# Performance work log

Hardware: AMD Instinct MI355X
Metric: run time of the kernel (lower is better)

Reference implementation:

```python
import jax, jax.numpy as jnp
import numpy as np

B, S, H, NH = 2, 2048, 1024, 16
HD = H // NH  # head_size = 64


def setup_inputs() -> dict:
    key = jax.random.key(0)
    ks = jax.random.split(key, 9)
    sc = 0.02
    return {
        "hidden_states": jax.random.normal(ks[0], (B, S, H), dtype=jnp.float32),
        "Wq": jax.random.normal(ks[1], (H, H), dtype=jnp.float32) * sc,
        "bq": jax.random.normal(ks[2], (H,), dtype=jnp.float32) * sc,
        "Wk": jax.random.normal(ks[3], (H, H), dtype=jnp.float32) * sc,
        "bk": jax.random.normal(ks[4], (H,), dtype=jnp.float32) * sc,
        "Wv": jax.random.normal(ks[5], (H, H), dtype=jnp.float32) * sc,
        "bv": jax.random.normal(ks[6], (H,), dtype=jnp.float32) * sc,
        "Wo": jax.random.normal(ks[7], (H, H), dtype=jnp.float32) * sc,
        "bo": jax.random.normal(ks[8], (H,), dtype=jnp.float32) * sc,
    }


def reference(hidden_states, Wq, bq, Wk, bk, Wv, bv, Wo, bo):
    b, s, h = hidden_states.shape
    # nn.Linear: y = x @ W.T + b
    q = hidden_states @ Wq.T + bq
    k = hidden_states @ Wk.T + bk
    v = hidden_states @ Wv.T + bv
    q = q.reshape(b, s, NH, HD)
    k = k.reshape(b, s, NH, HD)
    v = v.reshape(b, s, NH, HD)
    # scores: [b, heads, q, k]
    scores = jnp.einsum("bqhd,bkhd->bhqk", q, k) / jnp.sqrt(jnp.float32(HD))
    # causal mask: triu(ones, diagonal=1) positions set to -inf
    causal = jnp.triu(jnp.ones((s, s), dtype=bool), k=1)
    scores = jnp.where(causal[None, None], -jnp.inf, scores)
    attn = jax.nn.softmax(scores, axis=-1)
    ctx = jnp.einsum("bhqk,bkhd->bqhd", attn, v).reshape(b, s, h)
    return ctx @ Wo.T + bo
```

## Files before the change

kernel.cpp:

```cpp
#include <hip/hip_runtime.h>
#include <hip/hip_bf16.h>

#define B_  2
#define S_  2048
#define H_  1024
#define NH_ 16
#define HD_ 64

typedef unsigned short u16;
typedef unsigned int   u32;
typedef __attribute__((ext_vector_type(4)))  float  f32x4;
typedef __attribute__((ext_vector_type(16))) float  f32x16;
typedef __attribute__((ext_vector_type(8)))  __bf16 bf16x8;
typedef __attribute__((ext_vector_type(4)))  unsigned int u32x4;
typedef __attribute__((ext_vector_type(4)))  unsigned short u16x4;

__device__ __forceinline__ u16 f2bf(float f) {
  unsigned u = __builtin_bit_cast(unsigned, f);
  u += 0x7fffu + ((u >> 16) & 1u);
  return (u16)(u >> 16);
}
__device__ __forceinline__ u32 cvtpk(float lo, float hi) {
  u32 r;
  asm("v_cvt_pk_bf16_f32 %0, %1, %2" : "=v"(r) : "v"(lo), "v"(hi));
  return r;
}
__device__ __forceinline__ float ex2(float x) {
  float r;
  asm("v_exp_f32 %0, %1" : "=v"(r) : "v"(x));
  return r;
}

__device__ __forceinline__ void gload_lds16(const void* g, void* l) {
  __builtin_amdgcn_global_load_lds(
      (const __attribute__((address_space(1))) void*)g,
      (__attribute__((address_space(3))) void*)l, 16, 0, 0);
}

#define NX_ (4u * 1024u * 1024u)
__global__ __launch_bounds__(256) void cvt_all(const float* __restrict__ x,
                                               const float* __restrict__ w0, const float* __restrict__ w1,
                                               const float* __restrict__ w2, const float* __restrict__ w3,
                                               u16* __restrict__ xb,
                                               u16* __restrict__ o0, u16* __restrict__ o1,
                                               u16* __restrict__ o2, u16* __restrict__ o3) {
  size_t i4 = ((size_t)blockIdx.x * 256 + threadIdx.x) * 4;
  const float* src; u16* dst; size_t off;
  if (i4 < (size_t)NX_) { src = x; dst = xb; off = i4; }
  else {
    size_t j = i4 - NX_;
    int seg = (int)(j >> 20);
    off = j & ((1u << 20) - 1);
    src = seg == 0 ? w0 : seg == 1 ? w1 : seg == 2 ? w2 : w3;
    dst = seg == 0 ? o0 : seg == 1 ? o1 : seg == 2 ? o2 : o3;
  }
  float4 v = *reinterpret_cast<const float4*>(src + off);
  u16x4 o;
  o[0] = f2bf(v.x); o[1] = f2bf(v.y); o[2] = f2bf(v.z); o[3] = f2bf(v.w);
  *reinterpret_cast<u16x4*>(dst + off) = o;
}

__device__ __forceinline__ void store_out(float* C, size_t idx, float v) { C[idx] = v; }
__device__ __forceinline__ void store_out(u16* C, size_t idx, float v) { C[idx] = f2bf(v); }

template <int MI, typename OutT>
__device__ __forceinline__ void gemm_core(const u16* __restrict__ A, const u16* __restrict__ Bw,
                                          const float* __restrict__ bias, OutT* __restrict__ C,
                                          int M, int N, int K, float oscale, int m0, int n0,
                                          u16* lsA, u16* lsB) {
  const int t = threadIdx.x;
  const int w = t >> 6, lane = t & 63;
  const int g = lane >> 4, c = lane & 15;
  const int wr = w >> 1, wc = w & 1;

  f32x4 acc[MI][4] = {};
  const int rowS = w * 16 + (lane >> 2);
  const int colS = (lane & 3) * 8;

  for (int k0 = 0; k0 < K; k0 += 32) {
    __syncthreads();
#pragma unroll
    for (int r = 0; r < MI / 2; ++r)
      gload_lds16(A + (size_t)(m0 + r * 64 + rowS) * K + k0 + colS, lsA + r * 2048 + w * 512);
#pragma unroll
    for (int r = 0; r < 2; ++r)
      gload_lds16(Bw + (size_t)(n0 + r * 64 + rowS) * K + k0 + colS, lsB + r * 2048 + w * 512);
    asm volatile("s_waitcnt vmcnt(0)" ::: "memory");
    __syncthreads();

    bf16x8 af[MI], bfr[4];
#pragma unroll
    for (int mi = 0; mi < MI; ++mi)
      af[mi] = *reinterpret_cast<const bf16x8*>(&lsA[(wr * (MI * 16) + mi * 16 + c) * 32 + g * 8]);
#pragma unroll
    for (int ni = 0; ni < 4; ++ni)
      bfr[ni] = *reinterpret_cast<const bf16x8*>(&lsB[(wc * 64 + ni * 16 + c) * 32 + g * 8]);
#pragma unroll
    for (int mi = 0; mi < MI; ++mi)
#pragma unroll
      for (int ni = 0; ni < 4; ++ni)
        acc[mi][ni] = __builtin_amdgcn_mfma_f32_16x16x32_bf16(af[mi], bfr[ni], acc[mi][ni], 0, 0, 0);
  }

#pragma unroll
  for (int mi = 0; mi < MI; ++mi) {
    int rowb = m0 + wr * (MI * 16) + mi * 16 + g * 4;
#pragma unroll
    for (int ni = 0; ni < 4; ++ni) {
      int col = n0 + wc * 64 + ni * 16 + c;
      float bv = bias[col];
#pragma unroll
      for (int r = 0; r < 4; ++r) {
        float v = (acc[mi][ni][r] + bv) * oscale;
        store_out(C, (size_t)(rowb + r) * N + col, v);
      }
    }
  }
}

__global__ __launch_bounds__(256) void gemm_qkv(const u16* __restrict__ xb,
                                                const u16* __restrict__ Wq, const u16* __restrict__ Wk,
                                                const u16* __restrict__ Wv,
                                                const float* __restrict__ bq, const float* __restrict__ bk,
                                                const float* __restrict__ bv,
                                                u16* __restrict__ Q, u16* __restrict__ Kb, u16* __restrict__ Vb,
                                                int M, int K, float qscale) {
  __shared__ u16 lsA[4096];
  __shared__ u16 lsB[4096];
  const int fid = blockIdx.x;
  const int xcd = fid & 7, i = fid >> 3;
  const int mloc = i / 24, nn = i % 24;
  const int m0 = (xcd * 4 + mloc) * 128;
  const int ng = nn * 128;
  const int sel = ng >> 10, n0 = ng & 1023;
  const u16*  W    = sel == 0 ? Wq : sel == 1 ? Wk : Wv;
  const float* bia = sel == 0 ? bq : sel == 1 ? bk : bv;
  u16*        Cp   = sel == 0 ? Q  : sel == 1 ? Kb : Vb;
  float os = sel == 0 ? qscale : 1.0f;
  gemm_core<4, u16>(xb, W, bia, Cp, M, 1024, K, os, m0, n0, lsA, lsB);
}

__global__ __launch_bounds__(256) void gemm_wo(const u16* __restrict__ A, const u16* __restrict__ Bw,
                                               const float* __restrict__ bias, float* __restrict__ C,
                                               int M, int N, int K) {
  __shared__ u16 lsA[2048];
  __shared__ u16 lsB[4096];
  const int fid = blockIdx.x;
  const int xcd = fid & 7, i = fid >> 3;
  const int mloc = i >> 3, nn = i & 7;
  const int m0 = (xcd * 8 + mloc) * 64;
  const int n0 = nn * 128;
  gemm_core<2, float>(A, Bw, bias, C, M, N, K, 1.0f, m0, n0, lsA, lsB);
}

__global__ __launch_bounds__(256, 4) void attn_fwd(const u16* __restrict__ Qg,
                                                   const u16* __restrict__ Kg,
                                                   const u16* __restrict__ Vg,
                                                   u16* __restrict__ Og) {
  __shared__ __align__(16) u16 smem[18432];
  u16* lsKb = smem;
  u16* lsVb = smem + 8192;
  float* lsO  = (float*)smem;
  float* lsML = (float*)((char*)smem + 20480);
  u16*   lsOT = smem + 10752;

  const int blk = blockIdx.x;
  const int xcd = blk & 7, i = blk >> 3;
  const int j5 = i & 31, bgrp = i >> 5;
  const int qt = 31 - ((j5 + 8 * bgrp) & 31);
  const int bh = xcd * 4 + bgrp;
  const int h = bh & 15, b = bh >> 4;

  const int t = threadIdx.x, w = t >> 6, lane = t & 63;
  const int c5 = lane & 31, hi = lane >> 5;
  const int sub = w & 1, par = w >> 1;
  const size_t headoff = (size_t)b * (S_ * H_) + (size_t)h * HD_;
  const int q0w = qt * 64 + 32 * sub;

  const int sp = w & 1, sh = w >> 1;
  const int kRowLoc = 16 * sh + (lane >> 3);
  const int kSrcCol = ((lane & 7) ^ (lane >> 3)) << 4;
  const int vKvLoc  = 16 * sh + 2 * (lane >> 3);
  const int vD0     = 8 * (lane & 7);
  const int vKvx    = vKvLoc ^ (((lane & 7) & 3) << 3);

  int qkOff[4];
#pragma unroll
  for (int kc = 0; kc < 4; ++kc)
    qkOff[kc] = c5 * 128 + ((32 * kc + 16 * hi) ^ ((c5 & 7) << 4));
  const int pvRow0 = c5 * 80, pvRow1 = (32 + c5) * 80;
  int pvCol[2];
#pragma unroll
  for (int kp2 = 0; kp2 < 2; ++kp2)
    pvCol[kp2] = 2 * ((16 * kp2 + 8 * hi) ^ ((c5 >> 3) << 3));

  bf16x8 aq[4];
#pragma unroll
  for (int kc = 0; kc < 4; ++kc)
    aq[kc] = *reinterpret_cast<const bf16x8*>(Qg + headoff + (size_t)(q0w + c5) * H_ + kc * 16 + hi * 8);

  f32x16 o0 = {}, o1 = {};
  float mrun = -1e30f, lrun = 0.f;
  u32x4 vA, vB;

  auto STAGE = [&](int m) {
    const int kv0 = m * 64 + 32 * sp;
    const u16* vp = Vg + headoff + (size_t)(kv0 + vKvLoc) * H_ + vD0;
    vA = *reinterpret_cast<const u32x4*>(vp);
    vB = *reinterpret_cast<const u32x4*>(vp + H_);
    char* kt = (char*)(lsKb + ((m & 1) * 2 + sp) * 2048) + 16 * sh * 128;
    const char* ks = (const char*)(Kg + headoff + (size_t)(kv0 + kRowLoc) * H_) + kSrcCol;
    gload_lds16(ks, kt);
    gload_lds16(ks + 8 * (H_ * 2), kt + 8 * 128);
  };
  auto WRITEVT = [&](int m) {
    u16* vt = lsVb + ((m & 1) * 2 + sp) * 2560;
#pragma unroll
    for (int jj = 0; jj < 4; ++jj) {
      u32 lo  = __builtin_amdgcn_perm(vB[jj], vA[jj], 0x05040100u);
      u32 hi2 = __builtin_amdgcn_perm(vB[jj], vA[jj], 0x07060302u);
      *reinterpret_cast<u32*>(vt + (vD0 + 2 * jj) * 40 + vKvx)     = lo;
      *reinterpret_cast<u32*>(vt + (vD0 + 2 * jj + 1) * 40 + vKvx) = hi2;
    }
  };

  STAGE(0);
  asm volatile("s_waitcnt vmcnt(2)" ::: "memory");
  WRITEVT(0);
  asm volatile("s_waitcnt lgkmcnt(0)" ::: "memory");
  asm volatile("s_waitcnt vmcnt(0)" ::: "memory");
  __builtin_amdgcn_s_barrier();

  for (int n = 0; n <= qt; ++n) {
    const int buf = n & 1;
    const bool st = n < qt;
    if (st) STAGE(n + 1);

    const bool live = (2 * n + par) <= (2 * qt + sub);
    const bool diag = (2 * n + par) == (2 * qt + sub);
    f32x16 sc = {};
    if (live) {
      const char* kb = (const char*)(lsKb + (buf * 2 + par) * 2048);
      __builtin_amdgcn_s_setprio(1);
#pragma unroll
      for (int kc = 0; kc < 4; ++kc) {
        bf16x8 ak = *reinterpret_cast<const bf16x8*>(kb + qkOff[kc]);
        sc = __builtin_amdgcn_mfma_f32_32x32x16_bf16(ak, aq[kc], sc, 0, 0, 0);
      }
      __builtin_amdgcn_s_setprio(0);
      if (diag) {
#pragma unroll
        for (int r = 0; r < 16; ++r) {
          int kvl = (r & 3) + 8 * (r >> 2) + 4 * hi;
          sc[r] = (kvl > c5) ? -1e30f : sc[r];
        }
      }
      float pm = sc[0];
#pragma unroll
      for (int r = 1; r < 16; ++r) pm = fmaxf(pm, sc[r]);
      pm = fmaxf(pm, (float)__shfl_xor(pm, 32));
      if (!__all(pm <= mrun + 8.0f)) {
        float mn = fmaxf(mrun, pm);
        float s8 = ex2(mrun - mn);
        mrun = mn; lrun *= s8;
#pragma unroll
        for (int r = 0; r < 16; ++r) { o0[r] *= s8; o1[r] *= s8; }
      }
    }

    if (st) {
      asm volatile("s_waitcnt vmcnt(2)" ::: "memory");
      WRITEVT(n + 1);
    }

    if (live) {
      const char* vtb = (const char*)(lsVb + (buf * 2 + par) * 2560);
      float rs = 0.f;
      u32 wd0[2], wd1[2], wd2[2], wd3[2];
#pragma unroll
      for (int a = 0; a < 4; ++a) {
        float p0 = ex2(sc[4 * a + 0] - mrun), p1 = ex2(sc[4 * a + 1] - mrun);
        float p2 = ex2(sc[4 * a + 2] - mrun), p3 = ex2(sc[4 * a + 3] - mrun);
        rs += (p0 + p1) + (p2 + p3);
        u32* wdp = a == 0 ? wd0 : a == 1 ? wd1 : a == 2 ? wd2 : wd3;
        wdp[0] = cvtpk(p0, p1);
        wdp[1] = cvtpk(p2, p3);
      }
      rs += (float)__shfl_xor(rs, 32);
      lrun += rs;
      __builtin_amdgcn_s_setprio(1);
#pragma unroll
      for (int kp2 = 0; kp2 < 2; ++kp2) {
        u32 wa0 = kp2 ? wd2[0] : wd0[0], wa1 = kp2 ? wd2[1] : wd0[1];
        u32 wb0 = kp2 ? wd3[0] : wd1[0], wb1 = kp2 ? wd3[1] : wd1[1];
        u32 own0 = hi ? wb0 : wa0, own1 = hi ? wb1 : wa1;
        u32 snd0 = hi ? wa0 : wb0, snd1 = hi ? wa1 : wb1;
        u32 oth0 = (u32)__shfl_xor((int)snd0, 32);
        u32 oth1 = (u32)__shfl_xor((int)snd1, 32);
        u32x4 pw;
        pw[0] = hi ? oth0 : own0;
        pw[1] = hi ? oth1 : own1;
        pw[2] = hi ? own0 : oth0;
        pw[3] = hi ? own1 : oth1;
        bf16x8 pb = __builtin_bit_cast(bf16x8, pw);
        bf16x8 av0 = *reinterpret_cast<const bf16x8*>(vtb + pvRow0 + pvCol[kp2]);
        bf16x8 av1 = *reinterpret_cast<const bf16x8*>(vtb + pvRow1 + pvCol[kp2]);
        o0 = __builtin_amdgcn_mfma_f32_32x32x16_bf16(av0, pb, o0, 0, 0, 0);
        o1 = __builtin_amdgcn_mfma_f32_32x32x16_bf16(av1, pb, o1, 0, 0, 0);
      }
      __builtin_amdgcn_s_setprio(0);
    }

    asm volatile("s_waitcnt lgkmcnt(0)" ::: "memory");
    if (st) asm volatile("s_waitcnt vmcnt(0)" ::: "memory");
    __builtin_amdgcn_s_barrier();
  }

  if (par == 0) {
    if (hi == 0) { lsML[sub * 64 + c5] = mrun; lsML[sub * 64 + 32 + c5] = lrun; }
#pragma unroll
    for (int dt = 0; dt < 2; ++dt) {
      float* dst = lsO + ((size_t)((sub * 2 + dt) * 64 + lane)) * 20;
      const f32x16& oo = dt ? o1 : o0;
#pragma unroll
      for (int k4 = 0; k4 < 4; ++k4) {
        f32x4 v4 = {oo[4 * k4], oo[4 * k4 + 1], oo[4 * k4 + 2], oo[4 * k4 + 3]};
        *reinterpret_cast<f32x4*>(dst + 4 * k4) = v4;
      }
    }
  }
  __syncthreads();
  if (par == 1) {
    float mA = lsML[sub * 64 + c5];
    float lA = lsML[sub * 64 + 32 + c5];
    float mn = fmaxf(mA, mrun);
    float sA = ex2(mA - mn), sB = ex2(mrun - mn);
    float linv = 1.0f / (lA * sA + lrun * sB);
    sA *= linv; sB *= linv;
    u16* ot = lsOT + sub * 2304;
#pragma unroll
    for (int dt = 0; dt < 2; ++dt) {
      const float* sp2 = lsO + ((size_t)((sub * 2 + dt) * 64 + lane)) * 20;
      f32x4 a4[4];
#pragma unroll
      for (int k4 = 0; k4 < 4; ++k4) a4[k4] = *reinterpret_cast<const f32x4*>(sp2 + 4 * k4);
      const f32x16& oo = dt ? o1 : o0;
#pragma unroll
      for (int a = 0; a < 4; ++a)
#pragma unroll
        for (int u = 0; u < 2; ++u) {
          int r = 4 * a + 2 * u;
          float e0 = a4[a][2 * u]     * sA + oo[r]     * sB;
          float e1 = a4[a][2 * u + 1] * sA + oo[r + 1] * sB;
          int d = 32 * dt + 8 * a + 4 * hi + 2 * u;
          *reinterpret_cast<u32*>(ot + c5 * 72 + d) = cvtpk(e0, e1);
        }
    }
    asm volatile("s_waitcnt lgkmcnt(0)" ::: "memory");
    __builtin_amdgcn_sched_barrier(0);
#pragma unroll
    for (int rr = 0; rr < 4; ++rr) {
      int q = 8 * rr + (lane >> 3);
      int d8 = (lane & 7) * 8;
      u32x4 vv = *reinterpret_cast<const u32x4*>(ot + q * 72 + d8);
      *reinterpret_cast<u32x4*>(Og + headoff + (size_t)(qt * 64 + 32 * sub + q) * H_ + d8) = vv;
    }
  }
}

extern "C" void kernel_launch(void* const* d_in, const int* in_sizes, int n_in,
                              void* d_out, int out_size, void* d_ws, size_t ws_size,
                              hipStream_t stream) {
  const float* x  = (const float*)d_in[0];
  const float* Wq = (const float*)d_in[1];
  const float* bq = (const float*)d_in[2];
  const float* Wk = (const float*)d_in[3];
  const float* bk = (const float*)d_in[4];
  const float* Wv = (const float*)d_in[5];
  const float* bv = (const float*)d_in[6];
  const float* Wo = (const float*)d_in[7];
  const float* bo = (const float*)d_in[8];
  float* out = (float*)d_out;

  const size_t MT = (size_t)B_ * S_;
  char* p = (char*)d_ws;
  u16* xb  = (u16*)p; p += MT * H_ * 2;
  u16* Wqb = (u16*)p; p += (size_t)H_ * H_ * 2;
  u16* Wkb = (u16*)p; p += (size_t)H_ * H_ * 2;
  u16* Wvb = (u16*)p; p += (size_t)H_ * H_ * 2;
  u16* Wob = (u16*)p; p += (size_t)H_ * H_ * 2;
  u16* Qb  = (u16*)p; p += MT * H_ * 2;
  u16* Kb  = (u16*)p; p += MT * H_ * 2;
  u16* Vb  = (u16*)p; p += MT * H_ * 2;
  u16* Cb  = xb;

  cvt_all<<<8192, 256, 0, stream>>>(x, Wq, Wk, Wv, Wo, xb, Wqb, Wkb, Wvb, Wob);

  const float qscale = 0.125f * 1.44269504088896f;
  gemm_qkv<<<768, 256, 0, stream>>>(xb, Wqb, Wkb, Wvb, bq, bk, bv,
                                    Qb, Kb, Vb, (int)MT, H_, qscale);

  attn_fwd<<<1024, 256, 0, stream>>>(Qb, Kb, Vb, Cb);

  gemm_wo<<<512, 256, 0, stream>>>(Cb, Wob, bo, out, (int)MT, H_, H_);
}
```

Before: 114.6 us.

## Double-buffer GEMM LDS tiles and pair causal attention q-tiles per block

```diff
diff --git a/kernel.cpp b/kernel.cpp
--- a/kernel.cpp
+++ b/kernel.cpp
@@ -72,34 +72,51 @@
   const int w = t >> 6, lane = t & 63;
   const int g = lane >> 4, c = lane & 15;
   const int wr = w >> 1, wc = w & 1;
+  const int ABUF = MI * 1024, BBUF = 4096;
 
   f32x4 acc[MI][4] = {};
   const int rowS = w * 16 + (lane >> 2);
   const int colS = (lane & 3) * 8;
 
+  auto STAGE = [&](int k0, int buf) {
+#pragma unroll
+    for (int r = 0; r < MI / 2; ++r)
+      gload_lds16(A + (size_t)(m0 + r * 64 + rowS) * K + k0 + colS,
+                  lsA + buf * ABUF + r * 2048 + w * 512);
+#pragma unroll
+    for (int r = 0; r < 2; ++r)
+      gload_lds16(Bw + (size_t)(n0 + r * 64 + rowS) * K + k0 + colS,
+                  lsB + buf * BBUF + r * 2048 + w * 512);
+  };
+
+  STAGE(0, 0);
+  asm volatile("s_waitcnt vmcnt(0)" ::: "memory");
+  __builtin_amdgcn_s_barrier();
+
   for (int k0 = 0; k0 < K; k0 += 32) {
-    __syncthreads();
-#pragma unroll
-    for (int r = 0; r < MI / 2; ++r)
-      gload_lds16(A + (size_t)(m0 + r * 64 + rowS) * K + k0 + colS, lsA + r * 2048 + w * 512);
-#pragma unroll
-    for (int r = 0; r < 2; ++r)
-      gload_lds16(Bw + (size_t)(n0 + r * 64 + rowS) * K + k0 + colS, lsB + r * 2048 + w * 512);
-    asm volatile("s_waitcnt vmcnt(0)" ::: "memory");
-    __syncthreads();
+    const int cur = (k0 >> 5) & 1;
+    const bool st = (k0 + 32 < K);
+    if (st) STAGE(k0 + 32, cur ^ 1);
 
     bf16x8 af[MI], bfr[4];
 #pragma unroll
     for (int mi = 0; mi < MI; ++mi)
-      af[mi] = *reinterpret_cast<const bf16x8*>(&lsA[(wr * (MI * 16) + mi * 16 + c) * 32 + g * 8]);
+      af[mi] = *reinterpret_cast<const bf16x8*>(
+          &lsA[cur * ABUF + (wr * (MI * 16) + mi * 16 + c) * 32 + g * 8]);
 #pragma unroll
     for (int ni = 0; ni < 4; ++ni)
-      bfr[ni] = *reinterpret_cast<const bf16x8*>(&lsB[(wc * 64 + ni * 16 + c) * 32 + g * 8]);
+      bfr[ni] = *reinterpret_cast<const bf16x8*>(
+          &lsB[cur * BBUF + (wc * 64 + ni * 16 + c) * 32 + g * 8]);
 #pragma unroll
     for (int mi = 0; mi < MI; ++mi)
 #pragma unroll
       for (int ni = 0; ni < 4; ++ni)
         acc[mi][ni] = __builtin_amdgcn_mfma_f32_16x16x32_bf16(af[mi], bfr[ni], acc[mi][ni], 0, 0, 0);
+
+    if (st) {
+      asm volatile("s_waitcnt vmcnt(0)" ::: "memory");
+      __builtin_amdgcn_s_barrier();
+    }
   }
 
 #pragma unroll
@@ -125,8 +142,8 @@
                                                 const float* __restrict__ bv,
                                                 u16* __restrict__ Q, u16* __restrict__ Kb, u16* __restrict__ Vb,
                                                 int M, int K, float qscale) {
-  __shared__ u16 lsA[4096];
-  __shared__ u16 lsB[4096];
+  __shared__ u16 lsA[2 * 4096];
+  __shared__ u16 lsB[2 * 4096];
   const int fid = blockIdx.x;
   const int xcd = fid & 7, i = fid >> 3;
   const int mloc = i / 24, nn = i % 24;
@@ -143,8 +160,8 @@
 __global__ __launch_bounds__(256) void gemm_wo(const u16* __restrict__ A, const u16* __restrict__ Bw,
                                                const float* __restrict__ bias, float* __restrict__ C,
                                                int M, int N, int K) {
-  __shared__ u16 lsA[2048];
-  __shared__ u16 lsB[4096];
+  __shared__ u16 lsA[2 * 2048];
+  __shared__ u16 lsB[2 * 4096];
   const int fid = blockIdx.x;
   const int xcd = fid & 7, i = fid >> 3;
   const int mloc = i >> 3, nn = i & 7;
@@ -166,8 +183,7 @@
 
   const int blk = blockIdx.x;
   const int xcd = blk & 7, i = blk >> 3;
-  const int j5 = i & 31, bgrp = i >> 5;
-  const int qt = 31 - ((j5 + 8 * bgrp) & 31);
+  const int pj = i & 15, bgrp = i >> 4;
   const int bh = xcd * 4 + bgrp;
   const int h = bh & 15, b = bh >> 4;
 
@@ -175,7 +191,6 @@
   const int c5 = lane & 31, hi = lane >> 5;
   const int sub = w & 1, par = w >> 1;
   const size_t headoff = (size_t)b * (S_ * H_) + (size_t)h * HD_;
-  const int q0w = qt * 64 + 32 * sub;
 
   const int sp = w & 1, sh = w >> 1;
   const int kRowLoc = 16 * sh + (lane >> 3);
@@ -194,15 +209,7 @@
   for (int kp2 = 0; kp2 < 2; ++kp2)
     pvCol[kp2] = 2 * ((16 * kp2 + 8 * hi) ^ ((c5 >> 3) << 3));
 
-  bf16x8 aq[4];
-#pragma unroll
-  for (int kc = 0; kc < 4; ++kc)
-    aq[kc] = *reinterpret_cast<const bf16x8*>(Qg + headoff + (size_t)(q0w + c5) * H_ + kc * 16 + hi * 8);
-
-  f32x16 o0 = {}, o1 = {};
-  float mrun = -1e30f, lrun = 0.f;
   u32x4 vA, vB;
-
   auto STAGE = [&](int m) {
     const int kv0 = m * 64 + 32 * sp;
     const u16* vp = Vg + headoff + (size_t)(kv0 + vKvLoc) * H_ + vD0;
@@ -224,146 +231,160 @@
     }
   };
 
-  STAGE(0);
-  asm volatile("s_waitcnt vmcnt(2)" ::: "memory");
-  WRITEVT(0);
-  asm volatile("s_waitcnt lgkmcnt(0)" ::: "memory");
-  asm volatile("s_waitcnt vmcnt(0)" ::: "memory");
-  __builtin_amdgcn_s_barrier();
-
-  for (int n = 0; n <= qt; ++n) {
-    const int buf = n & 1;
-    const bool st = n < qt;
-    if (st) STAGE(n + 1);
-
-    const bool live = (2 * n + par) <= (2 * qt + sub);
-    const bool diag = (2 * n + par) == (2 * qt + sub);
-    f32x16 sc = {};
-    if (live) {
-      const char* kb = (const char*)(lsKb + (buf * 2 + par) * 2048);
-      __builtin_amdgcn_s_setprio(1);
-#pragma unroll
-      for (int kc = 0; kc < 4; ++kc) {
-        bf16x8 ak = *reinterpret_cast<const bf16x8*>(kb + qkOff[kc]);
-        sc = __builtin_amdgcn_mfma_f32_32x32x16_bf16(ak, aq[kc], sc, 0, 0, 0);
-      }
-      __builtin_amdgcn_s_setprio(0);
-      if (diag) {
-#pragma unroll
-        for (int r = 0; r < 16; ++r) {
-          int kvl = (r & 3) + 8 * (r >> 2) + 4 * hi;
-          sc[r] = (kvl > c5) ? -1e30f : sc[r];
-        }
-      }
-      float pm = sc[0];
-#pragma unroll
-      for (int r = 1; r < 16; ++r) pm = fmaxf(pm, sc[r]);
-      pm = fmaxf(pm, (float)__shfl_xor(pm, 32));
-      if (!__all(pm <= mrun + 8.0f)) {
-        float mn = fmaxf(mrun, pm);
-        float s8 = ex2(mrun - mn);
-        mrun = mn; lrun *= s8;
-#pragma unroll
-        for (int r = 0; r < 16; ++r) { o0[r] *= s8; o1[r] *= s8; }
-      }
-    }
-
-    if (st) {
-      asm volatile("s_waitcnt vmcnt(2)" ::: "memory");
-      WRITEVT(n + 1);
-    }
-
-    if (live) {
-      const char* vtb = (const char*)(lsVb + (buf * 2 + par) * 2560);
-      float rs = 0.f;
-      u32 wd0[2], wd1[2], wd2[2], wd3[2];
-#pragma unroll
-      for (int a = 0; a < 4; ++a) {
-        float p0 = ex2(sc[4 * a + 0] - mrun), p1 = ex2(sc[4 * a + 1] - mrun);
-        float p2 = ex2(sc[4 * a + 2] - mrun), p3 = ex2(sc[4 * a + 3] - mrun);
-        rs += (p0 + p1) + (p2 + p3);
-        u32* wdp = a == 0 ? wd0 : a == 1 ? wd1 : a == 2 ? wd2 : wd3;
-        wdp[0] = cvtpk(p0, p1);
-        wdp[1] = cvtpk(p2, p3);
-      }
-      rs += (float)__shfl_xor(rs, 32);
-      lrun += rs;
-      __builtin_amdgcn_s_setprio(1);
-#pragma unroll
-      for (int kp2 = 0; kp2 < 2; ++kp2) {
-        u32 wa0 = kp2 ? wd2[0] : wd0[0], wa1 = kp2 ? wd2[1] : wd0[1];
-        u32 wb0 = kp2 ? wd3[0] : wd1[0], wb1 = kp2 ? wd3[1] : wd1[1];
-        u32 own0 = hi ? wb0 : wa0, own1 = hi ? wb1 : wa1;
-        u32 snd0 = hi ? wa0 : wb0, snd1 = hi ? wa1 : wb1;
-        u32 oth0 = (u32)__shfl_xor((int)snd0, 32);
-        u32 oth1 = (u32)__shfl_xor((int)snd1, 32);
-        u32x4 pw;
-        pw[0] = hi ? oth0 : own0;
-        pw[1] = hi ? oth1 : own1;
-        pw[2] = hi ? own0 : oth0;
-        pw[3] = hi ? own1 : oth1;
-        bf16x8 pb = __builtin_bit_cast(bf16x8, pw);
-        bf16x8 av0 = *reinterpret_cast<const bf16x8*>(vtb + pvRow0 + pvCol[kp2]);
-        bf16x8 av1 = *reinterpret_cast<const bf16x8*>(vtb + pvRow1 + pvCol[kp2]);
-        o0 = __builtin_amdgcn_mfma_f32_32x32x16_bf16(av0, pb, o0, 0, 0, 0);
-        o1 = __builtin_amdgcn_mfma_f32_32x32x16_bf16(av1, pb, o1, 0, 0, 0);
-      }
-      __builtin_amdgcn_s_setprio(0);
-    }
-
+  for (int seg = 0; seg < 2; ++seg) {
+    const int qt = seg ? pj : 31 - pj;
+    const int q0w = qt * 64 + 32 * sub;
+    if (seg) __syncthreads();
+
+    bf16x8 aq[4];
+#pragma unroll
+    for (int kc = 0; kc < 4; ++kc)
+      aq[kc] = *reinterpret_cast<const bf16x8*>(Qg + headoff + (size_t)(q0w + c5) * H_ + kc * 16 + hi * 8);
+
+    f32x16 o0 = {}, o1 = {};
+    float mrun = -1e30f, lrun = 0.f;
+
+    STAGE(0);
+    asm volatile("s_waitcnt vmcnt(2)" ::: "memory");
+    WRITEVT(0);
     asm volatile("s_waitcnt lgkmcnt(0)" ::: "memory");
-    if (st) asm volatile("s_waitcnt vmcnt(0)" ::: "memory");
+    asm volatile("s_waitcnt vmcnt(0)" ::: "memory");
     __builtin_amdgcn_s_barrier();
-  }
-
-  if (par == 0) {
-    if (hi == 0) { lsML[sub * 64 + c5] = mrun; lsML[sub * 64 + 32 + c5] = lrun; }
-#pragma unroll
-    for (int dt = 0; dt < 2; ++dt) {
-      float* dst = lsO + ((size_t)((sub * 2 + dt) * 64 + lane)) * 20;
-      const f32x16& oo = dt ? o1 : o0;
-#pragma unroll
-      for (int k4 = 0; k4 < 4; ++k4) {
-        f32x4 v4 = {oo[4 * k4], oo[4 * k4 + 1], oo[4 * k4 + 2], oo[4 * k4 + 3]};
-        *reinterpret_cast<f32x4*>(dst + 4 * k4) = v4;
-      }
-    }
-  }
-  __syncthreads();
-  if (par == 1) {
-    float mA = lsML[sub * 64 + c5];
-    float lA = lsML[sub * 64 + 32 + c5];
-    float mn = fmaxf(mA, mrun);
-    float sA = ex2(mA - mn), sB = ex2(mrun - mn);
-    float linv = 1.0f / (lA * sA + lrun * sB);
-    sA *= linv; sB *= linv;
-    u16* ot = lsOT + sub * 2304;
-#pragma unroll
-    for (int dt = 0; dt < 2; ++dt) {
-      const float* sp2 = lsO + ((size_t)((sub * 2 + dt) * 64 + lane)) * 20;
-      f32x4 a4[4];
-#pragma unroll
-      for (int k4 = 0; k4 < 4; ++k4) a4[k4] = *reinterpret_cast<const f32x4*>(sp2 + 4 * k4);
-      const f32x16& oo = dt ? o1 : o0;
-#pragma unroll
-      for (int a = 0; a < 4; ++a)
-#pragma unroll
-        for (int u = 0; u < 2; ++u) {
-          int r = 4 * a + 2 * u;
-          float e0 = a4[a][2 * u]     * sA + oo[r]     * sB;
-          float e1 = a4[a][2 * u + 1] * sA + oo[r + 1] * sB;
-          int d = 32 * dt + 8 * a + 4 * hi + 2 * u;
-          *reinterpret_cast<u32*>(ot + c5 * 72 + d) = cvtpk(e0, e1);
-        }
-    }
-    asm volatile("s_waitcnt lgkmcnt(0)" ::: "memory");
-    __builtin_amdgcn_sched_barrier(0);
-#pragma unroll
-    for (int rr = 0; rr < 4; ++rr) {
-      int q = 8 * rr + (lane >> 3);
-      int d8 = (lane & 7) * 8;
-      u32x4 vv = *reinterpret_cast<const u32x4*>(ot + q * 72 + d8);
-      *reinterpret_cast<u32x4*>(Og + headoff + (size_t)(qt * 64 + 32 * sub + q) * H_ + d8) = vv;
+
+    for (int n = 0; n <= qt; ++n) {
+      const int buf = n & 1;
+      const bool st = n < qt;
+      if (st) STAGE(n + 1);
+
+      const bool live = (2 * n + par) <= (2 * qt + sub);
+      const bool diag = (2 * n + par) == (2 * qt + sub);
+      f32x16 sc = {};
+      if (live) {
+        const char* kb = (const char*)(lsKb + (buf * 2 + par) * 2048);
+        __builtin_amdgcn_s_setprio(1);
+#pragma unroll
+        for (int kc = 0; kc < 4; ++kc) {
+          bf16x8 ak = *reinterpret_cast<const bf16x8*>(kb + qkOff[kc]);
+          sc = __builtin_amdgcn_mfma_f32_32x32x16_bf16(ak, aq[kc], sc, 0, 0, 0);
+        }
+        __builtin_amdgcn_s_setprio(0);
+        if (diag) {
+#pragma unroll
+          for (int r = 0; r < 16; ++r) {
+            int kvl = (r & 3) + 8 * (r >> 2) + 4 * hi;
+            sc[r] = (kvl > c5) ? -1e30f : sc[r];
+          }
+        }
+        float pm = sc[0];
+#pragma unroll
+        for (int r = 1; r < 16; ++r) pm = fmaxf(pm, sc[r]);
+        pm = fmaxf(pm, (float)__shfl_xor(pm, 32));
+        if (!__all(pm <= mrun + 8.0f)) {
+          float mn = fmaxf(mrun, pm);
+          float s8 = ex2(mrun - mn);
+          mrun = mn; lrun *= s8;
+#pragma unroll
+          for (int r = 0; r < 16; ++r) { o0[r] *= s8; o1[r] *= s8; }
+        }
+      }
+
+      if (st) {
+        asm volatile("s_waitcnt vmcnt(2)" ::: "memory");
+        WRITEVT(n + 1);
+      }
+
+      if (live) {
+        const char* vtb = (const char*)(lsVb + (buf * 2 + par) * 2560);
+        float rs = 0.f;
+        u32 wd0[2], wd1[2], wd2[2], wd3[2];
+#pragma unroll
+        for (int a = 0; a < 4; ++a) {
+          float p0 = ex2(sc[4 * a + 0] - mrun), p1 = ex2(sc[4 * a + 1] - mrun);
+          float p2 = ex2(sc[4 * a + 2] - mrun), p3 = ex2(sc[4 * a + 3] - mrun);
+          rs += (p0 + p1) + (p2 + p3);
+          u32* wdp = a == 0 ? wd0 : a == 1 ? wd1 : a == 2 ? wd2 : wd3;
+          wdp[0] = cvtpk(p0, p1);
+          wdp[1] = cvtpk(p2, p3);
+        }
+        rs += (float)__shfl_xor(rs, 32);
+        lrun += rs;
+        __builtin_amdgcn_s_setprio(1);
+#pragma unroll
+        for (int kp2 = 0; kp2 < 2; ++kp2) {
+          u32 wa0 = kp2 ? wd2[0] : wd0[0], wa1 = kp2 ? wd2[1] : wd0[1];
+          u32 wb0 = kp2 ? wd3[0] : wd1[0], wb1 = kp2 ? wd3[1] : wd1[1];
+          u32 own0 = hi ? wb0 : wa0, own1 = hi ? wb1 : wa1;
+          u32 snd0 = hi ? wa0 : wb0, snd1 = hi ? wa1 : wb1;
+          u32 oth0 = (u32)__shfl_xor((int)snd0, 32);
+          u32 oth1 = (u32)__shfl_xor((int)snd1, 32);
+          u32x4 pw;
+          pw[0] = hi ? oth0 : own0;
+          pw[1] = hi ? oth1 : own1;
+          pw[2] = hi ? own0 : oth0;
+          pw[3] = hi ? own1 : oth1;
+          bf16x8 pb = __builtin_bit_cast(bf16x8, pw);
+          bf16x8 av0 = *reinterpret_cast<const bf16x8*>(vtb + pvRow0 + pvCol[kp2]);
+          bf16x8 av1 = *reinterpret_cast<const bf16x8*>(vtb + pvRow1 + pvCol[kp2]);
+          o0 = __builtin_amdgcn_mfma_f32_32x32x16_bf16(av0, pb, o0, 0, 0, 0);
+          o1 = __builtin_amdgcn_mfma_f32_32x32x16_bf16(av1, pb, o1, 0, 0, 0);
+        }
+        __builtin_amdgcn_s_setprio(0);
+      }
+
+      asm volatile("s_waitcnt lgkmcnt(0)" ::: "memory");
+      if (st) asm volatile("s_waitcnt vmcnt(0)" ::: "memory");
+      __builtin_amdgcn_s_barrier();
+    }
+
+    if (par == 0) {
+      if (hi == 0) { lsML[sub * 64 + c5] = mrun; lsML[sub * 64 + 32 + c5] = lrun; }
+#pragma unroll
+      for (int dt = 0; dt < 2; ++dt) {
+        float* dst = lsO + ((size_t)((sub * 2 + dt) * 64 + lane)) * 20;
+        const f32x16& oo = dt ? o1 : o0;
+#pragma unroll
+        for (int k4 = 0; k4 < 4; ++k4) {
+          f32x4 v4 = {oo[4 * k4], oo[4 * k4 + 1], oo[4 * k4 + 2], oo[4 * k4 + 3]};
+          *reinterpret_cast<f32x4*>(dst + 4 * k4) = v4;
+        }
+      }
+    }
+    __syncthreads();
+    if (par == 1) {
+      float mA = lsML[sub * 64 + c5];
+      float lA = lsML[sub * 64 + 32 + c5];
+      float mn = fmaxf(mA, mrun);
+      float sA = ex2(mA - mn), sB = ex2(mrun - mn);
+      float linv = 1.0f / (lA * sA + lrun * sB);
+      sA *= linv; sB *= linv;
+      u16* ot = lsOT + sub * 2304;
+#pragma unroll
+      for (int dt = 0; dt < 2; ++dt) {
+        const float* sp2 = lsO + ((size_t)((sub * 2 + dt) * 64 + lane)) * 20;
+        f32x4 a4[4];
+#pragma unroll
+        for (int k4 = 0; k4 < 4; ++k4) a4[k4] = *reinterpret_cast<const f32x4*>(sp2 + 4 * k4);
+        const f32x16& oo = dt ? o1 : o0;
+#pragma unroll
+        for (int a = 0; a < 4; ++a)
+#pragma unroll
+          for (int u = 0; u < 2; ++u) {
+            int r = 4 * a + 2 * u;
+            float e0 = a4[a][2 * u]     * sA + oo[r]     * sB;
+            float e1 = a4[a][2 * u + 1] * sA + oo[r + 1] * sB;
+            int d = 32 * dt + 8 * a + 4 * hi + 2 * u;
+            *reinterpret_cast<u32*>(ot + c5 * 72 + d) = cvtpk(e0, e1);
+          }
+      }
+      asm volatile("s_waitcnt lgkmcnt(0)" ::: "memory");
+      __builtin_amdgcn_sched_barrier(0);
+#pragma unroll
+      for (int rr = 0; rr < 4; ++rr) {
+        int q = 8 * rr + (lane >> 3);
+        int d8 = (lane & 7) * 8;
+        u32x4 vv = *reinterpret_cast<const u32x4*>(ot + q * 72 + d8);
+        *reinterpret_cast<u32x4*>(Og + headoff + (size_t)(qt * 64 + 32 * sub + q) * H_ + d8) = vv;
+      }
     }
   }
 }
@@ -400,7 +421,7 @@
   gemm_qkv<<<768, 256, 0, stream>>>(xb, Wqb, Wkb, Wvb, bq, bk, bv,
                                     Qb, Kb, Vb, (int)MT, H_, qscale);
 
-  attn_fwd<<<1024, 256, 0, stream>>>(Qb, Kb, Vb, Cb);
+  attn_fwd<<<512, 256, 0, stream>>>(Qb, Kb, Vb, Cb);
 
   gemm_wo<<<512, 256, 0, stream>>>(Cb, Wob, bo, out, (int)MT, H_, H_);
 }
```

After: 145.7 us. +27.1%, slower.
